# Kernel optimization log

Measured on AMD Instinct MI355X. Metric: run time of the kernel, lower is better.

## Reference

```python
import jax, jax.numpy as jnp
import numpy as np

B, H, L, D = 2, 16, 2048, 128


def setup_inputs() -> dict:
    key = jax.random.key(0)
    kq, kk, kv = jax.random.split(key, 3)
    q = jax.random.normal(kq, (B, H, L, D), dtype=jnp.float32)
    k = jax.random.normal(kk, (B, H, L, D), dtype=jnp.float32)
    v = jax.random.normal(kv, (B, H, L, D), dtype=jnp.float32)
    return {"q": q, "k": k, "v": v}


def reference(q, k, v):
    # Causal prefill attention (flash_attn_varlen_func / SDPA is_causal=True path).
    # q, k, v: [B, H, L, D]; scale = 1/sqrt(D) as in the fallback and constructor.
    Lq = q.shape[2]
    Dh = q.shape[3]
    scale = 1.0 / jnp.sqrt(jnp.asarray(Dh, q.dtype))
    scores = jnp.einsum('bhqd,bhkd->bhqk', q, k) * scale  # [B,H,Lq,Lk]
    causal = jnp.tril(jnp.ones((Lq, Lq), dtype=bool))      # [Lq,Lk]
    scores = jnp.where(causal, scores, jnp.finfo(q.dtype).min)
    probs = jax.nn.softmax(scores, axis=-1)
    return jnp.einsum('bhqk,bhkd->bhqd', probs, v)          # [B,H,Lq,D]
```

## Files before the change

kernel.cpp:

```cpp
#include <hip/hip_runtime.h>
#include <hip/hip_bf16.h>
#include <stdint.h>


#define BB 2
#define HH 16
#define LL 2048
#define DD 128

typedef float f32x4 __attribute__((ext_vector_type(4)));
typedef __bf16 bf16x8 __attribute__((ext_vector_type(8)));
typedef __bf16 bf16x2t __attribute__((ext_vector_type(2)));

union Frag16 {
    uint4    u;
    bf16x8   b;
    uint16_t s[8];
    uint32_t w32[4];
};

__device__ inline uint32_t pk2bf(float x, float y) {
    bf16x2t v;
    v.x = (__bf16)x;
    v.y = (__bf16)y;
    return __builtin_bit_cast(uint32_t, v);
}

__device__ inline uint16_t f2bf(float x) {
    uint32_t u = __builtin_bit_cast(uint32_t, x);
    u += 0x7fffu + ((u >> 16) & 1u);
    return (uint16_t)(u >> 16);
}

__device__ inline float fast_exp2(float x) {
#if __has_builtin(__builtin_amdgcn_exp2f)
    return __builtin_amdgcn_exp2f(x);
#else
    return exp2f(x);
#endif
}

__device__ __forceinline__ void stage16(const uint4* g, uint4* l) {
    __builtin_amdgcn_global_load_lds(
        (const __attribute__((address_space(1))) unsigned int*)g,
        (__attribute__((address_space(3))) unsigned int*)l, 16, 0, 0);
}

__global__ __launch_bounds__(256) void conv_kv(
    const float* __restrict__ Kg, const float* __restrict__ Vg,
    uint4* __restrict__ Kf, uint4* __restrict__ Vf)
{
    const int bid = blockIdx.x;
    const int t   = threadIdx.x;
    if (bid < 2048) {
        const int unit = bid;
        #pragma unroll
        for (int i = 0; i < 2; ++i) {
            const int local = t + i * 256;
            const int tile  = unit * 2 + (local >> 8);
            const int c     = local & 255;
            const int ds = c >> 6, quad = (c >> 4) & 3, n16 = c & 15;
            const float* p = Kg + ((size_t)tile * 16 + n16) * DD + ds * 32 + quad * 8;
            float4 a = *(const float4*)p;
            float4 b = *(const float4*)(p + 4);
            Frag16 f;
            f.w32[0] = pk2bf(a.x, a.y); f.w32[1] = pk2bf(a.z, a.w);
            f.w32[2] = pk2bf(b.x, b.y); f.w32[3] = pk2bf(b.z, b.w);
            Kf[(size_t)tile * 256 + c] = f.u;
        }
    } else {
        const int g = bid - 2048;
        const int n16 = t & 15, dt = (t >> 4) & 7, quadH = t >> 7;
        #pragma unroll
        for (int qi = 0; qi < 2; ++qi) {
            const int quad = quadH + 2 * qi;
            const float* base = Vg + ((size_t)g * 32 + quad * 8) * DD + dt * 16 + n16;
            float v[8];
            #pragma unroll
            for (int j = 0; j < 8; ++j) v[j] = base[(size_t)j * DD];
            Frag16 f;
            f.w32[0] = pk2bf(v[0], v[1]); f.w32[1] = pk2bf(v[2], v[3]);
            f.w32[2] = pk2bf(v[4], v[5]); f.w32[3] = pk2bf(v[6], v[7]);
            Vf[(size_t)g * 512 + dt * 64 + quad * 16 + n16] = f.u;
        }
    }
}

__global__ __launch_bounds__(256, 2) void fa_main(
    const float* __restrict__ Qg, const uint4* __restrict__ Kf,
    const uint4* __restrict__ Vf, float* __restrict__ Og)
{
    __shared__ __align__(16) uint4 Klds[2][1024];
    __shared__ __align__(16) uint4 Vlds[2][1024];
    __shared__ __align__(16) uint16_t Plds[4][2][16 * 40];
    __shared__ float Lbuf[2][2][16];
    float* Obuf = (float*)Klds;

    const int tid   = threadIdx.x;
    const int lane  = tid & 63;
    const int w     = tid >> 6;
    const int n16   = lane & 15;
    const int quad  = lane >> 4;
    const int qh    = w & 1;
    const int kvway = w >> 1;

    const int i    = blockIdx.x;
    const int xcd  = i & 7;
    const int j    = i >> 3;
    const int pair = j & 15;
    const int bh   = xcd * 4 + (j >> 4);

    constexpr float kC   = 0.08838834764831845f * 1.4426950408889634f;
    constexpr float kOff = -16.0f * 1.4426950408889634f;

    float* Oh = Og + (size_t)bh * LL * DD;

    #pragma unroll
    for (int phase = 0; phase < 2; ++phase) {
        const int qtile = phase ? pair : 31 - pair;
        const int q0    = qtile * 64;
        const int qw0   = q0 + qh * 32;

        Frag16 qf[2][4];
        #pragma unroll
        for (int qt = 0; qt < 2; ++qt) {
            const float* qrow = Qg + ((size_t)bh * LL + qw0 + qt * 16 + n16) * DD;
            #pragma unroll
            for (int ds = 0; ds < 4; ++ds) {
                const int d0 = ds * 32 + quad * 8;
                float4 a = *(const float4*)(qrow + d0);
                float4 b = *(const float4*)(qrow + d0 + 4);
                qf[qt][ds].w32[0] = pk2bf(a.x, a.y); qf[qt][ds].w32[1] = pk2bf(a.z, a.w);
                qf[qt][ds].w32[2] = pk2bf(b.x, b.y); qf[qt][ds].w32[3] = pk2bf(b.z, b.w);
            }
        }

        f32x4 oacc[2][8];
        #pragma unroll
        for (int qt = 0; qt < 2; ++qt)
            #pragma unroll
            for (int dt = 0; dt < 8; ++dt) oacc[qt][dt] = (f32x4)0.0f;
        float lpart[2] = {0.0f, 0.0f};

        const int ns = qtile + 1;

        auto STAGE = [&](int t, int buf) {
            const uint4* kg = Kf + ((size_t)(bh * 128 + 4 * t) * 256) + w * 256 + lane;
            const uint4* vg = Vf + ((size_t)(bh * 64 + 2 * t) * 512) + w * 256 + lane;
            uint4* kd = &Klds[buf][w * 256];
            uint4* vd = &Vlds[buf][w * 256];
            #pragma unroll
            for (int c = 0; c < 4; ++c) {
                stage16(kg + c * 64, kd + c * 64);
                stage16(vg + c * 64, vd + c * 64);
            }
        };

        STAGE(0, 0);
        __syncthreads();

        int cur = 0;
        for (int s = 0; s < ns; ++s) {
            if (s + 1 < ns) STAGE(s + 1, cur ^ 1);

            const uint4* Kl = Klds[cur];
            const uint4* Vl = Vlds[cur];
            const int kv0 = (s << 6) + (kvway << 5);

            if (kv0 <= qw0 + 31) {
                Frag16 vf[8];
                #pragma unroll
                for (int dt = 0; dt < 8; ++dt) vf[dt].u = Vl[kvway * 512 + dt * 64 + lane];

                f32x4 sacc[2][2];
                #pragma unroll
                for (int qt = 0; qt < 2; ++qt)
                    #pragma unroll
                    for (int kt = 0; kt < 2; ++kt) sacc[qt][kt] = (f32x4)0.0f;
                #pragma unroll
                for (int kt = 0; kt < 2; ++kt) {
                    Frag16 kfr[4];
                    #pragma unroll
                    for (int ds = 0; ds < 4; ++ds)
                        kfr[ds].u = Kl[(kvway * 2 + kt) * 256 + ds * 64 + lane];
                    __builtin_amdgcn_s_setprio(1);
                    #pragma unroll
                    for (int qt = 0; qt < 2; ++qt)
                        #pragma unroll
                        for (int ds = 0; ds < 4; ++ds)
                            sacc[qt][kt] = __builtin_amdgcn_mfma_f32_16x16x32_bf16(
                                kfr[ds].b, qf[qt][ds].b, sacc[qt][kt], 0, 0, 0);
                    __builtin_amdgcn_s_setprio(0);
                }

                if (kv0 + 31 > qw0) {
                    #pragma unroll
                    for (int qt = 0; qt < 2; ++qt) {
                        const int qg_ = qw0 + qt * 16 + n16;
                        #pragma unroll
                        for (int kt = 0; kt < 2; ++kt) {
                            const int kvg = kv0 + kt * 16 + quad * 4;
                            #pragma unroll
                            for (int r = 0; r < 4; ++r)
                                if (kvg + r > qg_) sacc[qt][kt][r] = -1e30f;
                        }
                    }
                }

                #pragma unroll
                for (int qt = 0; qt < 2; ++qt) {
                    #pragma unroll
                    for (int kt = 0; kt < 2; ++kt) {
                        float p0 = fast_exp2(fmaf(sacc[qt][kt][0], kC, kOff));
                        float p1 = fast_exp2(fmaf(sacc[qt][kt][1], kC, kOff));
                        float p2 = fast_exp2(fmaf(sacc[qt][kt][2], kC, kOff));
                        float p3 = fast_exp2(fmaf(sacc[qt][kt][3], kC, kOff));
                        lpart[qt] += (p0 + p1) + (p2 + p3);
                        uint2 pw2;
                        pw2.x = pk2bf(p0, p1);
                        pw2.y = pk2bf(p2, p3);
                        *(uint2*)&Plds[w][qt][n16 * 40 + kt * 16 + quad * 4] = pw2;
                    }
                }

                #pragma unroll
                for (int qt = 0; qt < 2; ++qt) {
                    Frag16 pf;
                    pf.u = *(const uint4*)&Plds[w][qt][n16 * 40 + quad * 8];
                    __builtin_amdgcn_s_setprio(1);
                    #pragma unroll
                    for (int dt = 0; dt < 8; ++dt)
                        oacc[qt][dt] = __builtin_amdgcn_mfma_f32_16x16x32_bf16(
                            pf.b, vf[dt].b, oacc[qt][dt], 0, 0, 0);
                    __builtin_amdgcn_s_setprio(0);
                }
            }

            __syncthreads();
            cur ^= 1;
        }

        float lsum[2];
        #pragma unroll
        for (int qt = 0; qt < 2; ++qt) {
            float ls = lpart[qt];
            ls += __shfl_xor(ls, 16);
            ls += __shfl_xor(ls, 32);
            lsum[qt] = ls;
        }

        if (kvway == 1) {
            if (lane < 16) {
                Lbuf[qh][0][lane] = lsum[0];
                Lbuf[qh][1][lane] = lsum[1];
            }
            #pragma unroll
            for (int qt = 0; qt < 2; ++qt)
                #pragma unroll
                for (int dt = 0; dt < 8; ++dt)
                    #pragma unroll
                    for (int r = 0; r < 4; ++r)
                        Obuf[((qh * 2 + qt) * 16 + quad * 4 + r) * 128 + dt * 16 + n16] =
                            oacc[qt][dt][r];
        }
        __syncthreads();
        if (kvway == 0) {
            #pragma unroll
            for (int qt = 0; qt < 2; ++qt) {
                const float ls = lsum[qt] + Lbuf[qh][qt][n16];
                #pragma unroll
                for (int r = 0; r < 4; ++r) {
                    const float inv = 1.0f / __shfl(ls, quad * 4 + r);
                    const float* obr = &Obuf[((qh * 2 + qt) * 16 + quad * 4 + r) * 128 + n16];
                    float* orow = Oh + (size_t)(qw0 + qt * 16 + quad * 4 + r) * DD + n16;
                    #pragma unroll
                    for (int dt = 0; dt < 8; ++dt)
                        orow[dt * 16] = (oacc[qt][dt][r] + obr[dt * 16]) * inv;
                }
            }
        }
        __syncthreads();
    }
}

__global__ __launch_bounds__(256) void fa_fallback(
    const float* __restrict__ Qg, const float* __restrict__ Kg,
    const float* __restrict__ Vg, float* __restrict__ Og)
{
    __shared__ uint4 Klds[32 * 16];
    __shared__ uint4 Vlds[128 * 4];
    __shared__ __align__(16) uint16_t Plds[4][32 * 40];

    const int tid  = threadIdx.x;
    const int lane = tid & 63;
    const int w    = tid >> 6;
    const int n16  = lane & 15;
    const int quad = lane >> 4;

    const int bh     = blockIdx.y;
    const int q0     = (gridDim.x - 1 - blockIdx.x) * 128;
    const int q_base = q0 + w * 32;

    const size_t base = (size_t)bh * LL * DD;
    const float* Qh = Qg + base;
    const float* Kh = Kg + base;
    const float* Vh = Vg + base;
    float*       Oh = Og + base;

    constexpr float kC = 0.08838834764831845f * 1.4426950408889634f;

    Frag16 qf[2][4];
    #pragma unroll
    for (int qt = 0; qt < 2; ++qt) {
        const float* qrow = Qh + (size_t)(q_base + qt * 16 + n16) * DD;
        #pragma unroll
        for (int ds = 0; ds < 4; ++ds) {
            const int d0 = ds * 32 + quad * 8;
            float4 a = *(const float4*)(qrow + d0);
            float4 b = *(const float4*)(qrow + d0 + 4);
            Frag16 f;
            f.s[0] = f2bf(a.x); f.s[1] = f2bf(a.y); f.s[2] = f2bf(a.z); f.s[3] = f2bf(a.w);
            f.s[4] = f2bf(b.x); f.s[5] = f2bf(b.y); f.s[6] = f2bf(b.z); f.s[7] = f2bf(b.w);
            qf[qt][ds] = f;
        }
    }

    f32x4 oacc[2][8];
    #pragma unroll
    for (int qt = 0; qt < 2; ++qt)
        #pragma unroll
        for (int dt = 0; dt < 8; ++dt) oacc[qt][dt] = (f32x4)0.0f;
    float mrow[2] = {-1e30f, -1e30f};
    float lrow[2] = {0.0f, 0.0f};

    const int ntiles = q0 / 32 + 4;

    for (int t = 0; t < ntiles; ++t) {
        const int kv0 = t * 32;
        __syncthreads();
        #pragma unroll
        for (int iu = 0; iu < 2; ++iu) {
            const int cid = tid + iu * 256;
            const int r = cid >> 4, c = cid & 15;
            const float* src = Kh + (size_t)(kv0 + r) * DD + c * 8;
            float4 a = *(const float4*)src;
            float4 b = *(const float4*)(src + 4);
            Frag16 f;
            f.s[0] = f2bf(a.x); f.s[1] = f2bf(a.y); f.s[2] = f2bf(a.z); f.s[3] = f2bf(a.w);
            f.s[4] = f2bf(b.x); f.s[5] = f2bf(b.y); f.s[6] = f2bf(b.z); f.s[7] = f2bf(b.w);
            Klds[r * 16 + (c ^ (r & 7))] = f.u;
        }
        #pragma unroll
        for (int iu = 0; iu < 2; ++iu) {
            const int cid = tid + iu * 256;
            const int d = cid >> 2, ch = cid & 3;
            const float* src = Vh + (size_t)(kv0 + ch * 8) * DD + d;
            Frag16 f;
            #pragma unroll
            for (int j = 0; j < 8; ++j) f.s[j] = f2bf(src[(size_t)j * DD]);
            Vlds[d * 4 + (ch ^ ((d >> 1) & 3))] = f.u;
        }
        __syncthreads();

        if (kv0 > q_base + 31) continue;

        f32x4 sacc[2][2];
        #pragma unroll
        for (int kt = 0; kt < 2; ++kt)
            #pragma unroll
            for (int qt = 0; qt < 2; ++qt) sacc[kt][qt] = (f32x4)0.0f;

        #pragma unroll
        for (int ds = 0; ds < 4; ++ds) {
            Frag16 kfr[2];
            #pragma unroll
            for (int kt = 0; kt < 2; ++kt) {
                const int r = kt * 16 + n16;
                const int c = ds * 4 + quad;
                kfr[kt].u = Klds[r * 16 + (c ^ (r & 7))];
            }
            #pragma unroll
            for (int kt = 0; kt < 2; ++kt)
                #pragma unroll
                for (int qt = 0; qt < 2; ++qt)
                    sacc[kt][qt] = __builtin_amdgcn_mfma_f32_16x16x32_bf16(
                        kfr[kt].b, qf[qt][ds].b, sacc[kt][qt], 0, 0, 0);
        }

        if (kv0 + 31 > q_base) {
            #pragma unroll
            for (int kt = 0; kt < 2; ++kt) {
                const int kvg = kv0 + kt * 16 + quad * 4;
                #pragma unroll
                for (int qt = 0; qt < 2; ++qt) {
                    const int qg_ = q_base + qt * 16 + n16;
                    #pragma unroll
                    for (int r = 0; r < 4; ++r)
                        if (kvg + r > qg_) sacc[kt][qt][r] = -1e30f;
                }
            }
        }

        #pragma unroll
        for (int qt = 0; qt < 2; ++qt) {
            float mt = sacc[0][qt][0];
            #pragma unroll
            for (int kt = 0; kt < 2; ++kt)
                #pragma unroll
                for (int r = 0; r < 4; ++r) mt = fmaxf(mt, sacc[kt][qt][r]);
            mt = fmaxf(mt, __shfl_xor(mt, 16));
            mt = fmaxf(mt, __shfl_xor(mt, 32));
            const float mnew  = fmaxf(mrow[qt], mt);
            const float alpha = exp2f((mrow[qt] - mnew) * kC);
            mrow[qt] = mnew;

            float ls = 0.0f;
            uint16_t* prow = &Plds[w][(qt * 16 + n16) * 40];
            #pragma unroll
            for (int kt = 0; kt < 2; ++kt)
                #pragma unroll
                for (int r = 0; r < 4; ++r) {
                    const float p = exp2f((sacc[kt][qt][r] - mnew) * kC);
                    ls += p;
                    prow[kt * 16 + quad * 4 + r] = f2bf(p);
                }
            ls += __shfl_xor(ls, 16);
            ls += __shfl_xor(ls, 32);
            lrow[qt] = lrow[qt] * alpha + ls;

            #pragma unroll
            for (int r = 0; r < 4; ++r) {
                const float ar = __shfl(alpha, quad * 4 + r);
                #pragma unroll
                for (int dt = 0; dt < 8; ++dt) oacc[qt][dt][r] *= ar;
            }
        }

        Frag16 pfr[2];
        #pragma unroll
        for (int qt = 0; qt < 2; ++qt)
            pfr[qt].u = *(const uint4*)&Plds[w][(qt * 16 + n16) * 40 + quad * 8];
        #pragma unroll
        for (int dt = 0; dt < 8; ++dt) {
            const int d = dt * 16 + n16;
            Frag16 vfr;
            vfr.u = Vlds[d * 4 + (quad ^ ((d >> 1) & 3))];
            #pragma unroll
            for (int qt = 0; qt < 2; ++qt)
                oacc[qt][dt] = __builtin_amdgcn_mfma_f32_16x16x32_bf16(
                    pfr[qt].b, vfr.b, oacc[qt][dt], 0, 0, 0);
        }
    }

    #pragma unroll
    for (int qt = 0; qt < 2; ++qt) {
        #pragma unroll
        for (int r = 0; r < 4; ++r) {
            const float lr  = __shfl(lrow[qt], quad * 4 + r);
            const float inv = 1.0f / lr;
            const int row = q_base + qt * 16 + quad * 4 + r;
            float* orow = Oh + (size_t)row * DD + n16;
            #pragma unroll
            for (int dt = 0; dt < 8; ++dt)
                orow[dt * 16] = oacc[qt][dt][r] * inv;
        }
    }
}

extern "C" void kernel_launch(void* const* d_in, const int* in_sizes, int n_in,
                              void* d_out, int out_size, void* d_ws, size_t ws_size,
                              hipStream_t stream) {
    const float* q = (const float*)d_in[0];
    const float* k = (const float*)d_in[1];
    const float* v = (const float*)d_in[2];
    float* o = (float*)d_out;

    const size_t TENS = (size_t)BB * HH * LL * DD * 2;
    if (ws_size >= 2 * TENS) {
        uint4* Kf = (uint4*)d_ws;
        uint4* Vf = (uint4*)((char*)d_ws + TENS);
        conv_kv<<<dim3(4096), dim3(256), 0, stream>>>(k, v, Kf, Vf);
        fa_main<<<dim3(512), dim3(256), 0, stream>>>(q, Kf, Vf, o);
    } else {
        fa_fallback<<<dim3(16, BB * HH), dim3(256), 0, stream>>>(q, k, v, o);
    }
}
```

Before: 181.5 us.

## Fuse K/V bf16 conversion into attention kernel with register-staged prefetch

Removes the separate conv_kv pre-pass that wrote bf16 fragment-layout K/V to workspace. The main kernel now loads fp32 K/V straight from global into registers for the next tile, overlapping those loads with the current tile's compute, then converts to bf16 and writes the fragments to LDS before the barrier. This avoids a second kernel launch and a round trip through the workspace, at the cost of more fp32 global traffic per block (K/V are reread and reconverted by each query tile), higher register pressure from 64 staging values, and strided scalar V loads. The fallback kernel is dropped as well.

```diff
diff --git a/kernel.cpp b/kernel.cpp
--- a/kernel.cpp
+++ b/kernel.cpp
@@ -26,12 +26,6 @@
     return __builtin_bit_cast(uint32_t, v);
 }
 
-__device__ inline uint16_t f2bf(float x) {
-    uint32_t u = __builtin_bit_cast(uint32_t, x);
-    u += 0x7fffu + ((u >> 16) & 1u);
-    return (uint16_t)(u >> 16);
-}
-
 __device__ inline float fast_exp2(float x) {
 #if __has_builtin(__builtin_amdgcn_exp2f)
     return __builtin_amdgcn_exp2f(x);
@@ -40,55 +34,9 @@
 #endif
 }
 
-__device__ __forceinline__ void stage16(const uint4* g, uint4* l) {
-    __builtin_amdgcn_global_load_lds(
-        (const __attribute__((address_space(1))) unsigned int*)g,
-        (__attribute__((address_space(3))) unsigned int*)l, 16, 0, 0);
-}
-
-__global__ __launch_bounds__(256) void conv_kv(
-    const float* __restrict__ Kg, const float* __restrict__ Vg,
-    uint4* __restrict__ Kf, uint4* __restrict__ Vf)
-{
-    const int bid = blockIdx.x;
-    const int t   = threadIdx.x;
-    if (bid < 2048) {
-        const int unit = bid;
-        #pragma unroll
-        for (int i = 0; i < 2; ++i) {
-            const int local = t + i * 256;
-            const int tile  = unit * 2 + (local >> 8);
-            const int c     = local & 255;
-            const int ds = c >> 6, quad = (c >> 4) & 3, n16 = c & 15;
-            const float* p = Kg + ((size_t)tile * 16 + n16) * DD + ds * 32 + quad * 8;
-            float4 a = *(const float4*)p;
-            float4 b = *(const float4*)(p + 4);
-            Frag16 f;
-            f.w32[0] = pk2bf(a.x, a.y); f.w32[1] = pk2bf(a.z, a.w);
-            f.w32[2] = pk2bf(b.x, b.y); f.w32[3] = pk2bf(b.z, b.w);
-            Kf[(size_t)tile * 256 + c] = f.u;
-        }
-    } else {
-        const int g = bid - 2048;
-        const int n16 = t & 15, dt = (t >> 4) & 7, quadH = t >> 7;
-        #pragma unroll
-        for (int qi = 0; qi < 2; ++qi) {
-            const int quad = quadH + 2 * qi;
-            const float* base = Vg + ((size_t)g * 32 + quad * 8) * DD + dt * 16 + n16;
-            float v[8];
-            #pragma unroll
-            for (int j = 0; j < 8; ++j) v[j] = base[(size_t)j * DD];
-            Frag16 f;
-            f.w32[0] = pk2bf(v[0], v[1]); f.w32[1] = pk2bf(v[2], v[3]);
-            f.w32[2] = pk2bf(v[4], v[5]); f.w32[3] = pk2bf(v[6], v[7]);
-            Vf[(size_t)g * 512 + dt * 64 + quad * 16 + n16] = f.u;
-        }
-    }
-}
-
 __global__ __launch_bounds__(256, 2) void fa_main(
-    const float* __restrict__ Qg, const uint4* __restrict__ Kf,
-    const uint4* __restrict__ Vf, float* __restrict__ Og)
+    const float* __restrict__ Qg, const float* __restrict__ Kg,
+    const float* __restrict__ Vg, float* __restrict__ Og)
 {
     __shared__ __align__(16) uint4 Klds[2][1024];
     __shared__ __align__(16) uint4 Vlds[2][1024];
@@ -103,6 +51,8 @@
     const int quad  = lane >> 4;
     const int qh    = w & 1;
     const int kvway = w >> 1;
+    const int vg_   = w >> 1;
+    const int dtb   = (w & 1) * 4;
 
     const int i    = blockIdx.x;
     const int xcd  = i & 7;
@@ -113,7 +63,10 @@
     constexpr float kC   = 0.08838834764831845f * 1.4426950408889634f;
     constexpr float kOff = -16.0f * 1.4426950408889634f;
 
-    float* Oh = Og + (size_t)bh * LL * DD;
+    const size_t base = (size_t)bh * LL * DD;
+    const float* Kh = Kg + base;
+    const float* Vh = Vg + base;
+    float*       Oh = Og + base;
 
     #pragma unroll
     for (int phase = 0; phase < 2; ++phase) {
@@ -124,7 +77,7 @@
         Frag16 qf[2][4];
         #pragma unroll
         for (int qt = 0; qt < 2; ++qt) {
-            const float* qrow = Qg + ((size_t)bh * LL + qw0 + qt * 16 + n16) * DD;
+            const float* qrow = Qg + base + (size_t)(qw0 + qt * 16 + n16) * DD;
             #pragma unroll
             for (int ds = 0; ds < 4; ++ds) {
                 const int d0 = ds * 32 + quad * 8;
@@ -144,24 +97,52 @@
 
         const int ns = qtile + 1;
 
-        auto STAGE = [&](int t, int buf) {
-            const uint4* kg = Kf + ((size_t)(bh * 128 + 4 * t) * 256) + w * 256 + lane;
-            const uint4* vg = Vf + ((size_t)(bh * 64 + 2 * t) * 512) + w * 256 + lane;
-            uint4* kd = &Klds[buf][w * 256];
-            uint4* vd = &Vlds[buf][w * 256];
-            #pragma unroll
-            for (int c = 0; c < 4; ++c) {
-                stage16(kg + c * 64, kd + c * 64);
-                stage16(vg + c * 64, vd + c * 64);
-            }
+        float4 ks[8];
+        float  vs[32];
+
+        auto STAGE_LOAD = [&](int t) {
+            const float* kb = Kh + (size_t)((t << 6) + w * 16 + n16) * DD + quad * 8;
+            #pragma unroll
+            for (int ds = 0; ds < 4; ++ds) {
+                ks[2 * ds]     = *(const float4*)(kb + ds * 32);
+                ks[2 * ds + 1] = *(const float4*)(kb + ds * 32 + 4);
+            }
+            const float* vb = Vh + (size_t)((t << 6) + vg_ * 32 + quad * 8) * DD + n16;
+            #pragma unroll
+            for (int dt = 0; dt < 4; ++dt)
+                #pragma unroll
+                for (int jj = 0; jj < 8; ++jj)
+                    vs[dt * 8 + jj] = vb[(size_t)jj * DD + (dtb + dt) * 16];
         };
-
-        STAGE(0, 0);
+        auto STAGE_WRITE = [&](int buf) {
+            #pragma unroll
+            for (int ds = 0; ds < 4; ++ds) {
+                Frag16 f;
+                f.w32[0] = pk2bf(ks[2 * ds].x,     ks[2 * ds].y);
+                f.w32[1] = pk2bf(ks[2 * ds].z,     ks[2 * ds].w);
+                f.w32[2] = pk2bf(ks[2 * ds + 1].x, ks[2 * ds + 1].y);
+                f.w32[3] = pk2bf(ks[2 * ds + 1].z, ks[2 * ds + 1].w);
+                Klds[buf][w * 256 + ds * 64 + lane] = f.u;
+            }
+            #pragma unroll
+            for (int dt = 0; dt < 4; ++dt) {
+                Frag16 f;
+                f.w32[0] = pk2bf(vs[dt * 8 + 0], vs[dt * 8 + 1]);
+                f.w32[1] = pk2bf(vs[dt * 8 + 2], vs[dt * 8 + 3]);
+                f.w32[2] = pk2bf(vs[dt * 8 + 4], vs[dt * 8 + 5]);
+                f.w32[3] = pk2bf(vs[dt * 8 + 6], vs[dt * 8 + 7]);
+                Vlds[buf][vg_ * 512 + (dtb + dt) * 64 + lane] = f.u;
+            }
+        };
+
+        STAGE_LOAD(0);
+        STAGE_WRITE(0);
         __syncthreads();
 
         int cur = 0;
         for (int s = 0; s < ns; ++s) {
-            if (s + 1 < ns) STAGE(s + 1, cur ^ 1);
+            const bool pre = (s + 1 < ns);
+            if (pre) STAGE_LOAD(s + 1);
 
             const uint4* Kl = Klds[cur];
             const uint4* Vl = Vlds[cur];
@@ -236,6 +217,7 @@
                 }
             }
 
+            if (pre) STAGE_WRITE(cur ^ 1);
             __syncthreads();
             cur ^= 1;
         }
@@ -283,190 +265,6 @@
     }
 }
 
-__global__ __launch_bounds__(256) void fa_fallback(
-    const float* __restrict__ Qg, const float* __restrict__ Kg,
-    const float* __restrict__ Vg, float* __restrict__ Og)
-{
-    __shared__ uint4 Klds[32 * 16];
-    __shared__ uint4 Vlds[128 * 4];
-    __shared__ __align__(16) uint16_t Plds[4][32 * 40];
-
-    const int tid  = threadIdx.x;
-    const int lane = tid & 63;
-    const int w    = tid >> 6;
-    const int n16  = lane & 15;
-    const int quad = lane >> 4;
-
-    const int bh     = blockIdx.y;
-    const int q0     = (gridDim.x - 1 - blockIdx.x) * 128;
-    const int q_base = q0 + w * 32;
-
-    const size_t base = (size_t)bh * LL * DD;
-    const float* Qh = Qg + base;
-    const float* Kh = Kg + base;
-    const float* Vh = Vg + base;
-    float*       Oh = Og + base;
-
-    constexpr float kC = 0.08838834764831845f * 1.4426950408889634f;
-
-    Frag16 qf[2][4];
-    #pragma unroll
-    for (int qt = 0; qt < 2; ++qt) {
-        const float* qrow = Qh + (size_t)(q_base + qt * 16 + n16) * DD;
-        #pragma unroll
-        for (int ds = 0; ds < 4; ++ds) {
-            const int d0 = ds * 32 + quad * 8;
-            float4 a = *(const float4*)(qrow + d0);
-            float4 b = *(const float4*)(qrow + d0 + 4);
-            Frag16 f;
-            f.s[0] = f2bf(a.x); f.s[1] = f2bf(a.y); f.s[2] = f2bf(a.z); f.s[3] = f2bf(a.w);
-            f.s[4] = f2bf(b.x); f.s[5] = f2bf(b.y); f.s[6] = f2bf(b.z); f.s[7] = f2bf(b.w);
-            qf[qt][ds] = f;
-        }
-    }
-
-    f32x4 oacc[2][8];
-    #pragma unroll
-    for (int qt = 0; qt < 2; ++qt)
-        #pragma unroll
-        for (int dt = 0; dt < 8; ++dt) oacc[qt][dt] = (f32x4)0.0f;
-    float mrow[2] = {-1e30f, -1e30f};
-    float lrow[2] = {0.0f, 0.0f};
-
-    const int ntiles = q0 / 32 + 4;
-
-    for (int t = 0; t < ntiles; ++t) {
-        const int kv0 = t * 32;
-        __syncthreads();
-        #pragma unroll
-        for (int iu = 0; iu < 2; ++iu) {
-            const int cid = tid + iu * 256;
-            const int r = cid >> 4, c = cid & 15;
-            const float* src = Kh + (size_t)(kv0 + r) * DD + c * 8;
-            float4 a = *(const float4*)src;
-            float4 b = *(const float4*)(src + 4);
-            Frag16 f;
-            f.s[0] = f2bf(a.x); f.s[1] = f2bf(a.y); f.s[2] = f2bf(a.z); f.s[3] = f2bf(a.w);
-            f.s[4] = f2bf(b.x); f.s[5] = f2bf(b.y); f.s[6] = f2bf(b.z); f.s[7] = f2bf(b.w);
-            Klds[r * 16 + (c ^ (r & 7))] = f.u;
-        }
-        #pragma unroll
-        for (int iu = 0; iu < 2; ++iu) {
-            const int cid = tid + iu * 256;
-            const int d = cid >> 2, ch = cid & 3;
-            const float* src = Vh + (size_t)(kv0 + ch * 8) * DD + d;
-            Frag16 f;
-            #pragma unroll
-            for (int j = 0; j < 8; ++j) f.s[j] = f2bf(src[(size_t)j * DD]);
-            Vlds[d * 4 + (ch ^ ((d >> 1) & 3))] = f.u;
-        }
-        __syncthreads();
-
-        if (kv0 > q_base + 31) continue;
-
-        f32x4 sacc[2][2];
-        #pragma unroll
-        for (int kt = 0; kt < 2; ++kt)
-            #pragma unroll
-            for (int qt = 0; qt < 2; ++qt) sacc[kt][qt] = (f32x4)0.0f;
-
-        #pragma unroll
-        for (int ds = 0; ds < 4; ++ds) {
-            Frag16 kfr[2];
-            #pragma unroll
-            for (int kt = 0; kt < 2; ++kt) {
-                const int r = kt * 16 + n16;
-                const int c = ds * 4 + quad;
-                kfr[kt].u = Klds[r * 16 + (c ^ (r & 7))];
-            }
-            #pragma unroll
-            for (int kt = 0; kt < 2; ++kt)
-                #pragma unroll
-                for (int qt = 0; qt < 2; ++qt)
-                    sacc[kt][qt] = __builtin_amdgcn_mfma_f32_16x16x32_bf16(
-                        kfr[kt].b, qf[qt][ds].b, sacc[kt][qt], 0, 0, 0);
-        }
-
-        if (kv0 + 31 > q_base) {
-            #pragma unroll
-            for (int kt = 0; kt < 2; ++kt) {
-                const int kvg = kv0 + kt * 16 + quad * 4;
-                #pragma unroll
-                for (int qt = 0; qt < 2; ++qt) {
-                    const int qg_ = q_base + qt * 16 + n16;
-                    #pragma unroll
-                    for (int r = 0; r < 4; ++r)
-                        if (kvg + r > qg_) sacc[kt][qt][r] = -1e30f;
-                }
-            }
-        }
-
-        #pragma unroll
-        for (int qt = 0; qt < 2; ++qt) {
-            float mt = sacc[0][qt][0];
-            #pragma unroll
-            for (int kt = 0; kt < 2; ++kt)
-                #pragma unroll
-                for (int r = 0; r < 4; ++r) mt = fmaxf(mt, sacc[kt][qt][r]);
-            mt = fmaxf(mt, __shfl_xor(mt, 16));
-            mt = fmaxf(mt, __shfl_xor(mt, 32));
-            const float mnew  = fmaxf(mrow[qt], mt);
-            const float alpha = exp2f((mrow[qt] - mnew) * kC);
-            mrow[qt] = mnew;
-
-            float ls = 0.0f;
-            uint16_t* prow = &Plds[w][(qt * 16 + n16) * 40];
-            #pragma unroll
-            for (int kt = 0; kt < 2; ++kt)
-                #pragma unroll
-                for (int r = 0; r < 4; ++r) {
-                    const float p = exp2f((sacc[kt][qt][r] - mnew) * kC);
-                    ls += p;
-                    prow[kt * 16 + quad * 4 + r] = f2bf(p);
-                }
-            ls += __shfl_xor(ls, 16);
-            ls += __shfl_xor(ls, 32);
-            lrow[qt] = lrow[qt] * alpha + ls;
-
-            #pragma unroll
-            for (int r = 0; r < 4; ++r) {
-                const float ar = __shfl(alpha, quad * 4 + r);
-                #pragma unroll
-                for (int dt = 0; dt < 8; ++dt) oacc[qt][dt][r] *= ar;
-            }
-        }
-
-        Frag16 pfr[2];
-        #pragma unroll
-        for (int qt = 0; qt < 2; ++qt)
-            pfr[qt].u = *(const uint4*)&Plds[w][(qt * 16 + n16) * 40 + quad * 8];
-        #pragma unroll
-        for (int dt = 0; dt < 8; ++dt) {
-            const int d = dt * 16 + n16;
-            Frag16 vfr;
-            vfr.u = Vlds[d * 4 + (quad ^ ((d >> 1) & 3))];
-            #pragma unroll
-            for (int qt = 0; qt < 2; ++qt)
-                oacc[qt][dt] = __builtin_amdgcn_mfma_f32_16x16x32_bf16(
-                    pfr[qt].b, vfr.b, oacc[qt][dt], 0, 0, 0);
-        }
-    }
-
-    #pragma unroll
-    for (int qt = 0; qt < 2; ++qt) {
-        #pragma unroll
-        for (int r = 0; r < 4; ++r) {
-            const float lr  = __shfl(lrow[qt], quad * 4 + r);
-            const float inv = 1.0f / lr;
-            const int row = q_base + qt * 16 + quad * 4 + r;
-            float* orow = Oh + (size_t)row * DD + n16;
-            #pragma unroll
-            for (int dt = 0; dt < 8; ++dt)
-                orow[dt * 16] = oacc[qt][dt][r] * inv;
-        }
-    }
-}
-
 extern "C" void kernel_launch(void* const* d_in, const int* in_sizes, int n_in,
                               void* d_out, int out_size, void* d_ws, size_t ws_size,
                               hipStream_t stream) {
@@ -474,14 +272,7 @@
     const float* k = (const float*)d_in[1];
     const float* v = (const float*)d_in[2];
     float* o = (float*)d_out;
-
-    const size_t TENS = (size_t)BB * HH * LL * DD * 2;
-    if (ws_size >= 2 * TENS) {
-        uint4* Kf = (uint4*)d_ws;
-        uint4* Vf = (uint4*)((char*)d_ws + TENS);
-        conv_kv<<<dim3(4096), dim3(256), 0, stream>>>(k, v, Kf, Vf);
-        fa_main<<<dim3(512), dim3(256), 0, stream>>>(q, Kf, Vf, o);
-    } else {
-        fa_fallback<<<dim3(16, BB * HH), dim3(256), 0, stream>>>(q, k, v, o);
-    }
-}
+    (void)d_ws; (void)ws_size;
+
+    fa_main<<<dim3(512), dim3(256), 0, stream>>>(q, k, v, o);
+}
```

After: 213.3 us. +17.5%, slower.

## Software-pipeline attention loop so softmax of previous tile overlaps next QK

Applied to the files above, without the earlier changes.

The main KV loop is restructured into prologue, steady state and epilogue. Each iteration now runs the exp/softmax and P·V for the previous tile, and QK^T plus the V-fragment load for the current tile. The aim is to interleave the exponential VALU work with MFMA work from independent tiles and hide latency. In exchange, the score accumulators and V fragments stay live across iterations, which raises register pressure and may lower occupancy.

```diff
diff --git a/kernel.cpp b/kernel.cpp
--- a/kernel.cpp
+++ b/kernel.cpp
@@ -144,6 +144,9 @@
 
         const int ns = qtile + 1;
 
+        f32x4 sacc[2][2];
+        Frag16 vf[8];
+
         auto STAGE = [&](int t, int buf) {
             const uint4* kg = Kf + ((size_t)(bh * 128 + 4 * t) * 256) + w * 256 + lane;
             const uint4* vg = Vf + ((size_t)(bh * 64 + 2 * t) * 512) + w * 256 + lane;
@@ -155,89 +158,106 @@
                 stage16(vg + c * 64, vd + c * 64);
             }
         };
+        auto QK = [&](const uint4* Kl, int kv0) {
+            #pragma unroll
+            for (int qt = 0; qt < 2; ++qt)
+                #pragma unroll
+                for (int kt = 0; kt < 2; ++kt) sacc[qt][kt] = (f32x4)0.0f;
+            #pragma unroll
+            for (int kt = 0; kt < 2; ++kt) {
+                Frag16 kfr[4];
+                #pragma unroll
+                for (int ds = 0; ds < 4; ++ds)
+                    kfr[ds].u = Kl[(kvway * 2 + kt) * 256 + ds * 64 + lane];
+                __builtin_amdgcn_s_setprio(1);
+                #pragma unroll
+                for (int qt = 0; qt < 2; ++qt)
+                    #pragma unroll
+                    for (int ds = 0; ds < 4; ++ds)
+                        sacc[qt][kt] = __builtin_amdgcn_mfma_f32_16x16x32_bf16(
+                            kfr[ds].b, qf[qt][ds].b, sacc[qt][kt], 0, 0, 0);
+                __builtin_amdgcn_s_setprio(0);
+            }
+            if (kv0 + 31 > qw0) {
+                #pragma unroll
+                for (int qt = 0; qt < 2; ++qt) {
+                    const int qg_ = qw0 + qt * 16 + n16;
+                    #pragma unroll
+                    for (int kt = 0; kt < 2; ++kt) {
+                        const int kvg = kv0 + kt * 16 + quad * 4;
+                        #pragma unroll
+                        for (int r = 0; r < 4; ++r)
+                            if (kvg + r > qg_) sacc[qt][kt][r] = -1e30f;
+                    }
+                }
+            }
+        };
+        auto SOFTMAX = [&]() {
+            #pragma unroll
+            for (int qt = 0; qt < 2; ++qt) {
+                #pragma unroll
+                for (int kt = 0; kt < 2; ++kt) {
+                    float p0 = fast_exp2(fmaf(sacc[qt][kt][0], kC, kOff));
+                    float p1 = fast_exp2(fmaf(sacc[qt][kt][1], kC, kOff));
+                    float p2 = fast_exp2(fmaf(sacc[qt][kt][2], kC, kOff));
+                    float p3 = fast_exp2(fmaf(sacc[qt][kt][3], kC, kOff));
+                    lpart[qt] += (p0 + p1) + (p2 + p3);
+                    uint2 pw2;
+                    pw2.x = pk2bf(p0, p1);
+                    pw2.y = pk2bf(p2, p3);
+                    *(uint2*)&Plds[w][qt][n16 * 40 + kt * 16 + quad * 4] = pw2;
+                }
+            }
+        };
+        auto PV = [&]() {
+            #pragma unroll
+            for (int qt = 0; qt < 2; ++qt) {
+                Frag16 pf;
+                pf.u = *(const uint4*)&Plds[w][qt][n16 * 40 + quad * 8];
+                __builtin_amdgcn_s_setprio(1);
+                #pragma unroll
+                for (int dt = 0; dt < 8; ++dt)
+                    oacc[qt][dt] = __builtin_amdgcn_mfma_f32_16x16x32_bf16(
+                        pf.b, vf[dt].b, oacc[qt][dt], 0, 0, 0);
+                __builtin_amdgcn_s_setprio(0);
+            }
+        };
+        auto LOADV = [&](const uint4* Vl) {
+            #pragma unroll
+            for (int dt = 0; dt < 8; ++dt)
+                vf[dt].u = Vl[kvway * 512 + dt * 64 + lane];
+        };
 
         STAGE(0, 0);
         __syncthreads();
 
         int cur = 0;
-        for (int s = 0; s < ns; ++s) {
+        {
+            if (ns > 1) STAGE(1, 1);
+            const int kv0 = kvway << 5;
+            if (kv0 <= qw0 + 31) {
+                QK(Klds[0], kv0);
+                LOADV(Vlds[0]);
+            }
+            __syncthreads();
+            cur = 1;
+        }
+
+        for (int s = 1; s < ns; ++s) {
             if (s + 1 < ns) STAGE(s + 1, cur ^ 1);
-
-            const uint4* Kl = Klds[cur];
-            const uint4* Vl = Vlds[cur];
+            SOFTMAX();
             const int kv0 = (s << 6) + (kvway << 5);
-
-            if (kv0 <= qw0 + 31) {
-                Frag16 vf[8];
-                #pragma unroll
-                for (int dt = 0; dt < 8; ++dt) vf[dt].u = Vl[kvway * 512 + dt * 64 + lane];
-
-                f32x4 sacc[2][2];
-                #pragma unroll
-                for (int qt = 0; qt < 2; ++qt)
-                    #pragma unroll
-                    for (int kt = 0; kt < 2; ++kt) sacc[qt][kt] = (f32x4)0.0f;
-                #pragma unroll
-                for (int kt = 0; kt < 2; ++kt) {
-                    Frag16 kfr[4];
-                    #pragma unroll
-                    for (int ds = 0; ds < 4; ++ds)
-                        kfr[ds].u = Kl[(kvway * 2 + kt) * 256 + ds * 64 + lane];
-                    __builtin_amdgcn_s_setprio(1);
-                    #pragma unroll
-                    for (int qt = 0; qt < 2; ++qt)
-                        #pragma unroll
-                        for (int ds = 0; ds < 4; ++ds)
-                            sacc[qt][kt] = __builtin_amdgcn_mfma_f32_16x16x32_bf16(
-                                kfr[ds].b, qf[qt][ds].b, sacc[qt][kt], 0, 0, 0);
-                    __builtin_amdgcn_s_setprio(0);
-                }
-
-                if (kv0 + 31 > qw0) {
-                    #pragma unroll
-                    for (int qt = 0; qt < 2; ++qt) {
-                        const int qg_ = qw0 + qt * 16 + n16;
-                        #pragma unroll
-                        for (int kt = 0; kt < 2; ++kt) {
-                            const int kvg = kv0 + kt * 16 + quad * 4;
-                            #pragma unroll
-                            for (int r = 0; r < 4; ++r)
-                                if (kvg + r > qg_) sacc[qt][kt][r] = -1e30f;
-                        }
-                    }
-                }
-
-                #pragma unroll
-                for (int qt = 0; qt < 2; ++qt) {
-                    #pragma unroll
-                    for (int kt = 0; kt < 2; ++kt) {
-                        float p0 = fast_exp2(fmaf(sacc[qt][kt][0], kC, kOff));
-                        float p1 = fast_exp2(fmaf(sacc[qt][kt][1], kC, kOff));
-                        float p2 = fast_exp2(fmaf(sacc[qt][kt][2], kC, kOff));
-                        float p3 = fast_exp2(fmaf(sacc[qt][kt][3], kC, kOff));
-                        lpart[qt] += (p0 + p1) + (p2 + p3);
-                        uint2 pw2;
-                        pw2.x = pk2bf(p0, p1);
-                        pw2.y = pk2bf(p2, p3);
-                        *(uint2*)&Plds[w][qt][n16 * 40 + kt * 16 + quad * 4] = pw2;
-                    }
-                }
-
-                #pragma unroll
-                for (int qt = 0; qt < 2; ++qt) {
-                    Frag16 pf;
-                    pf.u = *(const uint4*)&Plds[w][qt][n16 * 40 + quad * 8];
-                    __builtin_amdgcn_s_setprio(1);
-                    #pragma unroll
-                    for (int dt = 0; dt < 8; ++dt)
-                        oacc[qt][dt] = __builtin_amdgcn_mfma_f32_16x16x32_bf16(
-                            pf.b, vf[dt].b, oacc[qt][dt], 0, 0, 0);
-                    __builtin_amdgcn_s_setprio(0);
-                }
-            }
-
+            const bool act = kv0 <= qw0 + 31;
+            if (act) QK(Klds[cur], kv0);
+            PV();
+            if (act) LOADV(Vlds[cur]);
             __syncthreads();
             cur ^= 1;
+        }
+
+        {
+            const int kv0 = ((ns - 1) << 6) + (kvway << 5);
+            if (kv0 <= qw0 + 31) { SOFTMAX(); PV(); }
         }
 
         float lsum[2];
```

New measurement: 177.9 us. -2.0%, faster.

## Compute softmax row sums via MFMA with ones, peel masked tile, transpose V through LDS

Applied to the files above, without the earlier changes.

The per-lane scalar accumulation of exp values is replaced by an extra MFMA that multiplies the bf16 P tile by a ones fragment, producing row sums in the MFMA output layout and removing the shuffle reduction at the end. The main loop is split so unmasked tiles run without the causal-mask branch and only the final tile is masked. Staging pointers are advanced incrementally instead of being recomputed. The V conversion kernel now loads coalesced rows into LDS and transposes there instead of issuing strided global reads. Row sums are now taken from bf16-rounded P, which matches what the P·V product uses but adds one MFMA per q-tile per step.

```diff
diff --git a/kernel.cpp b/kernel.cpp
--- a/kernel.cpp
+++ b/kernel.cpp
@@ -50,6 +50,7 @@
     const float* __restrict__ Kg, const float* __restrict__ Vg,
     uint4* __restrict__ Kf, uint4* __restrict__ Vf)
 {
+    __shared__ uint16_t T[32 * 136];
     const int bid = blockIdx.x;
     const int t   = threadIdx.x;
     if (bid < 2048) {
@@ -70,18 +71,31 @@
         }
     } else {
         const int g = bid - 2048;
-        const int n16 = t & 15, dt = (t >> 4) & 7, quadH = t >> 7;
-        #pragma unroll
-        for (int qi = 0; qi < 2; ++qi) {
-            const int quad = quadH + 2 * qi;
-            const float* base = Vg + ((size_t)g * 32 + quad * 8) * DD + dt * 16 + n16;
-            float v[8];
-            #pragma unroll
-            for (int j = 0; j < 8; ++j) v[j] = base[(size_t)j * DD];
+        const float* Vsrc = Vg + (size_t)g * 32 * DD;
+        const int row = t >> 3;
+        const int cg  = (t & 7) * 16;
+        #pragma unroll
+        for (int k = 0; k < 4; ++k) {
+            float4 a = *(const float4*)(Vsrc + (size_t)row * DD + cg + k * 4);
+            uint2 pw;
+            pw.x = pk2bf(a.x, a.y);
+            pw.y = pk2bf(a.z, a.w);
+            *(uint2*)&T[row * 136 + cg + k * 4] = pw;
+        }
+        __syncthreads();
+        #pragma unroll
+        for (int e2 = 0; e2 < 2; ++e2) {
+            const int e   = t + e2 * 256;
+            const int dt  = e >> 6;
+            const int rem = e & 63;
+            const int qd  = rem >> 4;
+            const int nn  = rem & 15;
+            const int col = dt * 16 + nn;
             Frag16 f;
-            f.w32[0] = pk2bf(v[0], v[1]); f.w32[1] = pk2bf(v[2], v[3]);
-            f.w32[2] = pk2bf(v[4], v[5]); f.w32[3] = pk2bf(v[6], v[7]);
-            Vf[(size_t)g * 512 + dt * 64 + quad * 16 + n16] = f.u;
+            #pragma unroll
+            for (int jj = 0; jj < 8; ++jj)
+                f.s[jj] = T[(qd * 8 + jj) * 136 + col];
+            Vf[(size_t)g * 512 + e] = f.u;
         }
     }
 }
@@ -115,6 +129,14 @@
 
     float* Oh = Og + (size_t)bh * LL * DD;
 
+    Frag16 onesf;
+    #pragma unroll
+    for (int z = 0; z < 8; ++z) onesf.s[z] = 0x3F80;
+
+    uint4* kld = &Klds[0][0];
+    uint4* vld = &Vlds[0][0];
+    const int woff = w * 256;
+
     #pragma unroll
     for (int phase = 0; phase < 2; ++phase) {
         const int qtile = phase ? pair : 31 - pair;
@@ -140,119 +162,116 @@
         for (int qt = 0; qt < 2; ++qt)
             #pragma unroll
             for (int dt = 0; dt < 8; ++dt) oacc[qt][dt] = (f32x4)0.0f;
-        float lpart[2] = {0.0f, 0.0f};
+        f32x4 lacc[2] = {(f32x4)0.0f, (f32x4)0.0f};
 
         const int ns = qtile + 1;
 
-        auto STAGE = [&](int t, int buf) {
-            const uint4* kg = Kf + ((size_t)(bh * 128 + 4 * t) * 256) + w * 256 + lane;
-            const uint4* vg = Vf + ((size_t)(bh * 64 + 2 * t) * 512) + w * 256 + lane;
-            uint4* kd = &Klds[buf][w * 256];
-            uint4* vd = &Vlds[buf][w * 256];
+        const uint4* kg = Kf + (size_t)(bh * 128) * 256 + woff + lane;
+        const uint4* vg = Vf + (size_t)(bh * 64) * 512 + woff + lane;
+
+        auto STAGE = [&](int bufoff) {
+            uint4* kd = kld + bufoff + woff;
+            uint4* vd = vld + bufoff + woff;
             #pragma unroll
             for (int c = 0; c < 4; ++c) {
                 stage16(kg + c * 64, kd + c * 64);
                 stage16(vg + c * 64, vd + c * 64);
             }
+            kg += 1024;
+            vg += 1024;
         };
 
-        STAGE(0, 0);
-        __syncthreads();
-
-        int cur = 0;
-        for (int s = 0; s < ns; ++s) {
-            if (s + 1 < ns) STAGE(s + 1, cur ^ 1);
-
-            const uint4* Kl = Klds[cur];
-            const uint4* Vl = Vlds[cur];
-            const int kv0 = (s << 6) + (kvway << 5);
-
-            if (kv0 <= qw0 + 31) {
-                Frag16 vf[8];
-                #pragma unroll
-                for (int dt = 0; dt < 8; ++dt) vf[dt].u = Vl[kvway * 512 + dt * 64 + lane];
-
-                f32x4 sacc[2][2];
+        auto COMPUTE = [&](int bufoff, bool masked, int kv0) {
+            const uint4* Kl = kld + bufoff + kvway * 512 + lane;
+            const uint4* Vl = vld + bufoff + kvway * 512 + lane;
+            Frag16 vf[8];
+            #pragma unroll
+            for (int dt = 0; dt < 8; ++dt) vf[dt].u = Vl[dt * 64];
+            f32x4 sacc[2][2];
+            #pragma unroll
+            for (int qt = 0; qt < 2; ++qt)
+                #pragma unroll
+                for (int kt = 0; kt < 2; ++kt) sacc[qt][kt] = (f32x4)0.0f;
+            #pragma unroll
+            for (int kt = 0; kt < 2; ++kt) {
+                Frag16 kfr[4];
+                #pragma unroll
+                for (int ds = 0; ds < 4; ++ds) kfr[ds].u = Kl[kt * 256 + ds * 64];
+                __builtin_amdgcn_s_setprio(1);
                 #pragma unroll
                 for (int qt = 0; qt < 2; ++qt)
                     #pragma unroll
-                    for (int kt = 0; kt < 2; ++kt) sacc[qt][kt] = (f32x4)0.0f;
-                #pragma unroll
-                for (int kt = 0; kt < 2; ++kt) {
-                    Frag16 kfr[4];
+                    for (int ds = 0; ds < 4; ++ds)
+                        sacc[qt][kt] = __builtin_amdgcn_mfma_f32_16x16x32_bf16(
+                            kfr[ds].b, qf[qt][ds].b, sacc[qt][kt], 0, 0, 0);
+                __builtin_amdgcn_s_setprio(0);
+            }
+            if (masked) {
+                #pragma unroll
+                for (int qt = 0; qt < 2; ++qt) {
+                    const int qg_ = qw0 + qt * 16 + n16;
                     #pragma unroll
-                    for (int ds = 0; ds < 4; ++ds)
-                        kfr[ds].u = Kl[(kvway * 2 + kt) * 256 + ds * 64 + lane];
-                    __builtin_amdgcn_s_setprio(1);
-                    #pragma unroll
-                    for (int qt = 0; qt < 2; ++qt)
+                    for (int kt = 0; kt < 2; ++kt) {
+                        const int kvg = kv0 + kt * 16 + quad * 4;
                         #pragma unroll
-                        for (int ds = 0; ds < 4; ++ds)
-                            sacc[qt][kt] = __builtin_amdgcn_mfma_f32_16x16x32_bf16(
-                                kfr[ds].b, qf[qt][ds].b, sacc[qt][kt], 0, 0, 0);
-                    __builtin_amdgcn_s_setprio(0);
-                }
-
-                if (kv0 + 31 > qw0) {
-                    #pragma unroll
-                    for (int qt = 0; qt < 2; ++qt) {
-                        const int qg_ = qw0 + qt * 16 + n16;
-                        #pragma unroll
-                        for (int kt = 0; kt < 2; ++kt) {
-                            const int kvg = kv0 + kt * 16 + quad * 4;
-                            #pragma unroll
-                            for (int r = 0; r < 4; ++r)
-                                if (kvg + r > qg_) sacc[qt][kt][r] = -1e30f;
-                        }
+                        for (int r = 0; r < 4; ++r)
+                            if (kvg + r > qg_) sacc[qt][kt][r] = -1e30f;
                     }
                 }
-
-                #pragma unroll
-                for (int qt = 0; qt < 2; ++qt) {
-                    #pragma unroll
-                    for (int kt = 0; kt < 2; ++kt) {
-                        float p0 = fast_exp2(fmaf(sacc[qt][kt][0], kC, kOff));
-                        float p1 = fast_exp2(fmaf(sacc[qt][kt][1], kC, kOff));
-                        float p2 = fast_exp2(fmaf(sacc[qt][kt][2], kC, kOff));
-                        float p3 = fast_exp2(fmaf(sacc[qt][kt][3], kC, kOff));
-                        lpart[qt] += (p0 + p1) + (p2 + p3);
-                        uint2 pw2;
-                        pw2.x = pk2bf(p0, p1);
-                        pw2.y = pk2bf(p2, p3);
-                        *(uint2*)&Plds[w][qt][n16 * 40 + kt * 16 + quad * 4] = pw2;
-                    }
+            }
+            #pragma unroll
+            for (int qt = 0; qt < 2; ++qt) {
+                uint16_t* pw = &Plds[w][qt][n16 * 40];
+                #pragma unroll
+                for (int kt = 0; kt < 2; ++kt) {
+                    float p0 = fast_exp2(fmaf(sacc[qt][kt][0], kC, kOff));
+                    float p1 = fast_exp2(fmaf(sacc[qt][kt][1], kC, kOff));
+                    float p2 = fast_exp2(fmaf(sacc[qt][kt][2], kC, kOff));
+                    float p3 = fast_exp2(fmaf(sacc[qt][kt][3], kC, kOff));
+                    uint2 pw2;
+                    pw2.x = pk2bf(p0, p1);
+                    pw2.y = pk2bf(p2, p3);
+                    *(uint2*)&pw[kt * 16 + quad * 4] = pw2;
                 }
-
-                #pragma unroll
-                for (int qt = 0; qt < 2; ++qt) {
-                    Frag16 pf;
-                    pf.u = *(const uint4*)&Plds[w][qt][n16 * 40 + quad * 8];
-                    __builtin_amdgcn_s_setprio(1);
-                    #pragma unroll
-                    for (int dt = 0; dt < 8; ++dt)
-                        oacc[qt][dt] = __builtin_amdgcn_mfma_f32_16x16x32_bf16(
-                            pf.b, vf[dt].b, oacc[qt][dt], 0, 0, 0);
-                    __builtin_amdgcn_s_setprio(0);
-                }
-            }
-
+            }
+            #pragma unroll
+            for (int qt = 0; qt < 2; ++qt) {
+                Frag16 pf;
+                pf.u = *(const uint4*)&Plds[w][qt][n16 * 40 + quad * 8];
+                __builtin_amdgcn_s_setprio(1);
+                lacc[qt] = __builtin_amdgcn_mfma_f32_16x16x32_bf16(
+                    pf.b, onesf.b, lacc[qt], 0, 0, 0);
+                #pragma unroll
+                for (int dt = 0; dt < 8; ++dt)
+                    oacc[qt][dt] = __builtin_amdgcn_mfma_f32_16x16x32_bf16(
+                        pf.b, vf[dt].b, oacc[qt][dt], 0, 0, 0);
+                __builtin_amdgcn_s_setprio(0);
+            }
+        };
+
+        STAGE(0);
+        __syncthreads();
+
+        int cur = 0;
+        for (int s = 0; s < ns - 1; ++s) {
+            STAGE((cur ^ 1) << 10);
+            COMPUTE(cur << 10, false, 0);
             __syncthreads();
             cur ^= 1;
         }
-
-        float lsum[2];
-        #pragma unroll
-        for (int qt = 0; qt < 2; ++qt) {
-            float ls = lpart[qt];
-            ls += __shfl_xor(ls, 16);
-            ls += __shfl_xor(ls, 32);
-            lsum[qt] = ls;
+        {
+            const int kv0 = ((ns - 1) << 6) + (kvway << 5);
+            if (kv0 <= qw0 + 31) COMPUTE(cur << 10, true, kv0);
+            __syncthreads();
         }
 
         if (kvway == 1) {
-            if (lane < 16) {
-                Lbuf[qh][0][lane] = lsum[0];
-                Lbuf[qh][1][lane] = lsum[1];
+            if (n16 == 0) {
+                #pragma unroll
+                for (int qt = 0; qt < 2; ++qt)
+                    #pragma unroll
+                    for (int r = 0; r < 4; ++r)
+                        Lbuf[qh][qt][quad * 4 + r] = lacc[qt][r];
             }
             #pragma unroll
             for (int qt = 0; qt < 2; ++qt)
@@ -267,10 +286,10 @@
         if (kvway == 0) {
             #pragma unroll
             for (int qt = 0; qt < 2; ++qt) {
-                const float ls = lsum[qt] + Lbuf[qh][qt][n16];
                 #pragma unroll
                 for (int r = 0; r < 4; ++r) {
-                    const float inv = 1.0f / __shfl(ls, quad * 4 + r);
+                    const float lt  = lacc[qt][r] + Lbuf[qh][qt][quad * 4 + r];
+                    const float inv = 1.0f / lt;
                     const float* obr = &Obuf[((qh * 2 + qt) * 16 + quad * 4 + r) * 128 + n16];
                     float* orow = Oh + (size_t)(qw0 + qt * 16 + quad * 4 + r) * DD + n16;
                     #pragma unroll
```

Result: no change. 179.3 us (-1.2%).
